# Performance work log

Measured on AMD Instinct MI355X. Metric: run time of the kernel, lower is better.

## Reference

```python
import jax, jax.numpy as jnp
import numpy as np
import math

D = 512      # d_model = sd_dim*2
DFF = 512    # dim_feedforward
S = 512      # num_seg (queries)
T = 32768    # video frames (keys)
RATE = 4     # self-attention band half-width
SCALE = 1.0 / math.sqrt(D)


def _ln(x, g, b):
    m = x.mean(-1, keepdims=True)
    v = ((x - m) ** 2).mean(-1, keepdims=True)
    return (x - m) / jnp.sqrt(v + 1e-5) * g + b


def setup_inputs() -> dict:
    key = jax.random.key(0)
    ks = jax.random.split(key, 12)
    w = lambda k, shp, s=0.02: jax.random.normal(k, shp, jnp.float32) * s
    # exactly S contiguous action segments over T frames
    action_idx = jnp.asarray((np.arange(T) * S) // T, dtype=jnp.int32)
    return dict(
        tgt=w(ks[0], (S, 1, D), 1.0), memory=w(ks[1], (T, 1, D), 1.0),
        pos=w(ks[2], (T, 1, D), 0.1), query_pos=w(ks[3], (S, 1, D), 0.1),
        action_idx=action_idx,
        ca_t2l_w=w(ks[4], (D, D)), ca_t2l_b=jnp.zeros(D),
        ca_l1_w=w(ks[5], (DFF, D)), ca_l1_b=jnp.zeros(DFF),
        ca_l2_w=w(ks[6], (D, DFF)), ca_l2_b=jnp.zeros(D),
        ca_n2_g=jnp.ones(D), ca_n2_b=jnp.zeros(D),
        ca_n3_g=jnp.ones(D), ca_n3_b=jnp.zeros(D),
        sa_conv_w=w(ks[7], (D, D)), sa_conv_b=jnp.zeros(D),
        sa_l1_w=w(ks[8], (DFF, D)), sa_l1_b=jnp.zeros(DFF),
        sa_l2_w=w(ks[9], (D, DFF)), sa_l2_b=jnp.zeros(D),
        sa_n1_g=jnp.ones(D), sa_n1_b=jnp.zeros(D),
        sa_n2_g=jnp.ones(D), sa_n2_b=jnp.zeros(D),
    )


def reference(tgt, memory, pos, query_pos, action_idx,
              ca_t2l_w, ca_t2l_b, ca_l1_w, ca_l1_b, ca_l2_w, ca_l2_b,
              ca_n2_g, ca_n2_b, ca_n3_g, ca_n3_b,
              sa_conv_w, sa_conv_b, sa_l1_w, sa_l1_b, sa_l2_w, sa_l2_b,
              sa_n1_g, sa_n1_b, sa_n2_g, sa_n2_b):
    # ---------------- CrossAttention (segment mask) ----------------
    q = tgt + query_pos                      # (S,1,D)
    k = memory + pos                         # (T,1,D)
    scores = jnp.einsum('sbd,tbd->bst', q, k) * SCALE   # (1,S,T)
    # segment id per frame from change points of action_idx
    chg = (action_idx[1:] != action_idx[:-1]).astype(jnp.int32)
    seg_id = jnp.concatenate([jnp.zeros(1, jnp.int32), jnp.cumsum(chg)])  # (T,)
    # query i attends to segments i-1, i, i+1
    mask = jnp.abs(seg_id[None, :] - jnp.arange(S, dtype=jnp.int32)[:, None]) <= 1  # (S,T)
    scores = jnp.where(mask[None], scores, -jnp.inf)
    attn = jax.nn.softmax(scores, axis=-1)               # (1,S,T)
    tgt2 = jnp.einsum('bst,tbd->sbd', attn, memory)      # (S,1,D)
    tgt2 = jnp.maximum(tgt2, 0.0) @ ca_t2l_w.T + ca_t2l_b
    x = _ln(tgt + tgt2, ca_n2_g, ca_n2_b)
    ffn = jnp.maximum(x @ ca_l1_w.T + ca_l1_b, 0.0) @ ca_l2_w.T + ca_l2_b
    x = _ln(x + ffn, ca_n3_g, ca_n3_b)                   # (S,1,D)
    # ---------------- SelfAttention (banded, pos=None) ----------------
    src = jnp.transpose(x, (1, 0, 2))                    # (1,S,D)
    s2 = jnp.einsum('bsd,btd->bst', src, src) * SCALE    # (1,S,S)
    i = jnp.arange(S)
    band = jnp.abs(i[:, None] - i[None, :]) <= RATE      # (S,S)
    s2 = jnp.where(band[None], s2, -jnp.inf)
    a2 = jax.nn.softmax(s2, axis=-1)                     # (1,S,S)
    src2 = jnp.einsum('bqk,bkd->bqd', a2, src)           # (1,S,D)
    src2 = jnp.maximum(src2, 0.0) @ sa_conv_w.T + sa_conv_b  # 1x1 conv over channels
    y = _ln(src + src2, sa_n1_g, sa_n1_b)
    ffn2 = jnp.maximum(y @ sa_l1_w.T + sa_l1_b, 0.0) @ sa_l2_w.T + sa_l2_b
    y = _ln(y + ffn2, sa_n2_g, sa_n2_b)
    return y                                              # (1,S,D)
```

## Files before the change

kernel.cpp:

```cpp
#include <hip/hip_runtime.h>

#define S_Q 512
#define DIM 512
#define SCALE_F 0.04419417382415922f

typedef short short8 __attribute__((ext_vector_type(8)));
typedef float floatx4 __attribute__((ext_vector_type(4)));

__device__ __forceinline__ float wave_reduce_sum(float v) {
#pragma unroll
  for (int off = 32; off > 0; off >>= 1) v += __shfl_xor(v, off);
  return v;
}

__device__ __forceinline__ unsigned short f2bf(float f) {
  unsigned int u = __float_as_uint(f);
  return (unsigned short)((u + 0x7FFFu + ((u >> 16) & 1u)) >> 16);
}

__global__ __launch_bounds__(256) void k_ca_partial(
    const float* __restrict__ tgt, const float* __restrict__ qpos,
    const float* __restrict__ mem, const float* __restrict__ pos,
    float* __restrict__ part_acc, float* __restrict__ part_ms) {
  const int j = blockIdx.x >> 1;
  const int h = blockIdx.x & 1;
  const int tid = threadIdx.x;
  const int wave = tid >> 6, lane = tid & 63;
  const int d0 = lane * 8;

  __shared__ float wacc[4][3][DIM];
  __shared__ float wms[4][3][2];

  float qf[3][8];
#pragma unroll
  for (int c = 0; c < 3; ++c) {
    const int qi = j - 1 + c;
    if ((unsigned)qi < (unsigned)S_Q) {
      const float4* tp = (const float4*)(tgt + (size_t)qi * DIM + d0);
      const float4* qp = (const float4*)(qpos + (size_t)qi * DIM + d0);
      float4 t0 = tp[0], t1 = tp[1], q0 = qp[0], q1 = qp[1];
      qf[c][0] = t0.x + q0.x; qf[c][1] = t0.y + q0.y;
      qf[c][2] = t0.z + q0.z; qf[c][3] = t0.w + q0.w;
      qf[c][4] = t1.x + q1.x; qf[c][5] = t1.y + q1.y;
      qf[c][6] = t1.z + q1.z; qf[c][7] = t1.w + q1.w;
    } else {
#pragma unroll
      for (int e = 0; e < 8; ++e) qf[c][e] = 0.f;
    }
  }

  float m[3] = {-1e30f, -1e30f, -1e30f};
  float ssum[3] = {0.f, 0.f, 0.f};
  float acc[3][8];
#pragma unroll
  for (int c = 0; c < 3; ++c)
#pragma unroll
    for (int e = 0; e < 8; ++e) acc[c][e] = 0.f;

  const size_t fbase = (size_t)j * 64 + h * 32 + wave * 8;
#pragma unroll 2
  for (int it = 0; it < 8; ++it) {
    const size_t f = fbase + it;
    const float4* mp = (const float4*)(mem + f * DIM + d0);
    const float4* pp = (const float4*)(pos + f * DIM + d0);
    float4 m0 = mp[0], m1 = mp[1], p0 = pp[0], p1 = pp[1];
    float mv[8] = {m0.x, m0.y, m0.z, m0.w, m1.x, m1.y, m1.z, m1.w};
    float kk[8] = {m0.x + p0.x, m0.y + p0.y, m0.z + p0.z, m0.w + p0.w,
                   m1.x + p1.x, m1.y + p1.y, m1.z + p1.z, m1.w + p1.w};
    float s0 = 0.f, s1 = 0.f, s2 = 0.f;
#pragma unroll
    for (int e = 0; e < 8; ++e) {
      s0 += qf[0][e] * kk[e];
      s1 += qf[1][e] * kk[e];
      s2 += qf[2][e] * kk[e];
    }
#pragma unroll
    for (int off = 32; off > 0; off >>= 1) {
      s0 += __shfl_xor(s0, off);
      s1 += __shfl_xor(s1, off);
      s2 += __shfl_xor(s2, off);
    }
    const float sc3[3] = {s0 * SCALE_F, s1 * SCALE_F, s2 * SCALE_F};
#pragma unroll
    for (int c = 0; c < 3; ++c) {
      const float s = sc3[c];
      if (s > m[c]) {
        const float fct = __expf(m[c] - s);
        ssum[c] = ssum[c] * fct + 1.f;
#pragma unroll
        for (int e = 0; e < 8; ++e) acc[c][e] = acc[c][e] * fct + mv[e];
        m[c] = s;
      } else {
        const float ee = __expf(s - m[c]);
        ssum[c] += ee;
#pragma unroll
        for (int e = 0; e < 8; ++e) acc[c][e] += ee * mv[e];
      }
    }
  }

#pragma unroll
  for (int c = 0; c < 3; ++c) {
    *(float4*)(&wacc[wave][c][d0]) =
        make_float4(acc[c][0], acc[c][1], acc[c][2], acc[c][3]);
    *(float4*)(&wacc[wave][c][d0 + 4]) =
        make_float4(acc[c][4], acc[c][5], acc[c][6], acc[c][7]);
    if (lane == 0) { wms[wave][c][0] = m[c]; wms[wave][c][1] = ssum[c]; }
  }
  __syncthreads();

  const int d = tid * 2;
#pragma unroll
  for (int c = 0; c < 3; ++c) {
    const int qi = j - 1 + c;
    if ((unsigned)qi >= (unsigned)S_Q) continue;
    float M = wms[0][c][0];
#pragma unroll
    for (int w = 1; w < 4; ++w) M = fmaxf(M, wms[w][c][0]);
    float S = 0.f, ax = 0.f, ay = 0.f;
#pragma unroll
    for (int w = 0; w < 4; ++w) {
      const float wgt = __expf(wms[w][c][0] - M);
      S += wgt * wms[w][c][1];
      const float2 a = *(const float2*)(&wacc[w][c][d]);
      ax += wgt * a.x;
      ay += wgt * a.y;
    }
    const size_t slot = (size_t)qi * 6 + c * 2 + h;
    *(float2*)(part_acc + slot * DIM + d) = make_float2(ax, ay);
    if (tid == 0) {
      part_ms[slot * 2 + 0] = M;
      part_ms[slot * 2 + 1] = S;
    }
  }
}

__global__ __launch_bounds__(256) void k_ca_combine(
    const float* __restrict__ part_acc, const float* __restrict__ part_ms,
    float* __restrict__ t2r) {
  const int i = blockIdx.x;
  const int tid = threadIdx.x;
  const bool valid[3] = {i < S_Q - 1, true, i > 0};
  float ms[6], ss[6];
  float M = -1e30f;
#pragma unroll
  for (int k = 0; k < 6; ++k) {
    if (valid[k >> 1]) {
      ms[k] = part_ms[((size_t)i * 6 + k) * 2 + 0];
      ss[k] = part_ms[((size_t)i * 6 + k) * 2 + 1];
      M = fmaxf(M, ms[k]);
    } else {
      ms[k] = -1e30f;
      ss[k] = 0.f;
    }
  }
  float wgt[6];
  float den = 0.f;
#pragma unroll
  for (int k = 0; k < 6; ++k) {
    wgt[k] = valid[k >> 1] ? __expf(ms[k] - M) : 0.f;
    den += wgt[k] * ss[k];
  }
  const float inv = 1.f / den;
  const int d = tid * 2;
  float ox = 0.f, oy = 0.f;
#pragma unroll
  for (int k = 0; k < 6; ++k) {
    if (valid[k >> 1]) {
      const float2 a = *(const float2*)(part_acc + ((size_t)i * 6 + k) * DIM + d);
      ox += wgt[k] * a.x;
      oy += wgt[k] * a.y;
    }
  }
  ox = fmaxf(ox * inv, 0.f);
  oy = fmaxf(oy * inv, 0.f);
  *(float2*)(t2r + (size_t)i * DIM + d) = make_float2(ox, oy);
}

template <bool RELU>
__global__ __launch_bounds__(256) void k_gemm512(
    const float* __restrict__ A, const float* __restrict__ W,
    const float* __restrict__ bias, float* __restrict__ C) {
  __shared__ short As[32 * 72];
  __shared__ short Ws[32 * 72];
  const int tid = threadIdx.x;
  const int bx = blockIdx.x, by = blockIdx.y;
  const int wave = tid >> 6, lane = tid & 63;
  const int srow = tid >> 3, sk = (tid & 7) * 4;
  const float* Ag = A + (size_t)(by * 32 + srow) * DIM + sk;
  const float* Wg = W + (size_t)(bx * 32 + srow) * DIM + sk;
  const int r0 = (wave >> 1) * 16, c0 = (wave & 1) * 16;
  const int frow = lane & 15, fk = (lane >> 4) * 8;
  floatx4 acc = {0.f, 0.f, 0.f, 0.f};
  for (int kc = 0; kc < DIM; kc += 32) {
    const float4 av = *(const float4*)(Ag + kc);
    const float4 wv = *(const float4*)(Wg + kc);
    __syncthreads();
    short* ap = &As[srow * 72 + sk];
    ap[0] = (short)f2bf(av.x); ap[1] = (short)f2bf(av.y);
    ap[2] = (short)f2bf(av.z); ap[3] = (short)f2bf(av.w);
    short* wp = &Ws[srow * 72 + sk];
    wp[0] = (short)f2bf(wv.x); wp[1] = (short)f2bf(wv.y);
    wp[2] = (short)f2bf(wv.z); wp[3] = (short)f2bf(wv.w);
    __syncthreads();
    const short8 af = *(const short8*)(&As[(r0 + frow) * 72 + fk]);
    const short8 wf = *(const short8*)(&Ws[(c0 + frow) * 72 + fk]);
    acc = __builtin_amdgcn_mfma_f32_16x16x32_bf16(af, wf, acc, 0, 0, 0);
  }
  const int col = bx * 32 + c0 + (lane & 15);
  const int rowb = by * 32 + r0 + (lane >> 4) * 4;
  const float b = bias[col];
#pragma unroll
  for (int r = 0; r < 4; ++r) {
    float val = acc[r] + b;
    if (RELU) val = fmaxf(val, 0.f);
    C[(size_t)(rowb + r) * DIM + col] = val;
  }
}

__global__ __launch_bounds__(256) void k_addln(
    const float* __restrict__ X, const float* __restrict__ R,
    const float* __restrict__ g, const float* __restrict__ b,
    float* __restrict__ out) {
  const int row = blockIdx.x * 4 + (threadIdx.x >> 6);
  const int lane = threadIdx.x & 63;
  const int d = lane * 8;
  const float4* xp = (const float4*)(X + (size_t)row * DIM + d);
  const float4* rp = (const float4*)(R + (size_t)row * DIM + d);
  float4 x0 = xp[0], x1 = xp[1], r0 = rp[0], r1 = rp[1];
  float v[8] = {x0.x + r0.x, x0.y + r0.y, x0.z + r0.z, x0.w + r0.w,
                x1.x + r1.x, x1.y + r1.y, x1.z + r1.z, x1.w + r1.w};
  float s = 0.f, sq = 0.f;
#pragma unroll
  for (int e = 0; e < 8; ++e) { s += v[e]; sq += v[e] * v[e]; }
  s = wave_reduce_sum(s);
  sq = wave_reduce_sum(sq);
  const float mean = s * (1.f / DIM);
  const float var = sq * (1.f / DIM) - mean * mean;
  const float rstd = rsqrtf(var + 1e-5f);
  const float4* gp = (const float4*)(g + d);
  const float4* bp = (const float4*)(b + d);
  float4 g0 = gp[0], g1 = gp[1], bb0 = bp[0], bb1 = bp[1];
  float4 o0, o1;
  o0.x = (v[0] - mean) * rstd * g0.x + bb0.x;
  o0.y = (v[1] - mean) * rstd * g0.y + bb0.y;
  o0.z = (v[2] - mean) * rstd * g0.z + bb0.z;
  o0.w = (v[3] - mean) * rstd * g0.w + bb0.w;
  o1.x = (v[4] - mean) * rstd * g1.x + bb1.x;
  o1.y = (v[5] - mean) * rstd * g1.y + bb1.y;
  o1.z = (v[6] - mean) * rstd * g1.z + bb1.z;
  o1.w = (v[7] - mean) * rstd * g1.w + bb1.w;
  *(float4*)(out + (size_t)row * DIM + d) = o0;
  *(float4*)(out + (size_t)row * DIM + d + 4) = o1;
}

__global__ __launch_bounds__(256) void k_sa_attn(const float* __restrict__ X,
                                                 float* __restrict__ outr) {
  const int i = blockIdx.x;
  const int tid = threadIdx.x;
  const int wave = tid >> 6, lane = tid & 63;
  const int jlo = (i - 4 > 0) ? i - 4 : 0;
  const int jhi = (i + 4 < S_Q - 1) ? i + 4 : S_Q - 1;
  const int n = jhi - jlo + 1;
  __shared__ float sc[9];
  const int d0 = lane * 8;
  const float4* qp = (const float4*)(X + (size_t)i * DIM + d0);
  float4 q0 = qp[0], q1 = qp[1];
  for (int idx = wave; idx < n; idx += 4) {
    const float4* kp = (const float4*)(X + (size_t)(jlo + idx) * DIM + d0);
    float4 k0 = kp[0], k1 = kp[1];
    float s = q0.x * k0.x + q0.y * k0.y + q0.z * k0.z + q0.w * k0.w +
              q1.x * k1.x + q1.y * k1.y + q1.z * k1.z + q1.w * k1.w;
    s = wave_reduce_sum(s);
    if (lane == 0) sc[idx] = s * SCALE_F;
  }
  __syncthreads();
  float m = -3.0e38f;
#pragma unroll
  for (int k = 0; k < 9; ++k)
    if (k < n) m = fmaxf(m, sc[k]);
  float p[9];
  float den = 0.f;
#pragma unroll
  for (int k = 0; k < 9; ++k) {
    p[k] = (k < n) ? __expf(sc[k] - m) : 0.f;
    den += p[k];
  }
  const float inv = 1.f / den;
  const int d = tid * 2;
  float ox = 0.f, oy = 0.f;
#pragma unroll
  for (int k = 0; k < 9; ++k) {
    if (k < n) {
      float2 xv = *(const float2*)(X + (size_t)(jlo + k) * DIM + d);
      ox += p[k] * xv.x;
      oy += p[k] * xv.y;
    }
  }
  ox = fmaxf(ox * inv, 0.f);
  oy = fmaxf(oy * inv, 0.f);
  *(float2*)(outr + (size_t)i * DIM + d) = make_float2(ox, oy);
}

extern "C" void kernel_launch(void* const* d_in, const int* in_sizes, int n_in,
                              void* d_out, int out_size, void* d_ws, size_t ws_size,
                              hipStream_t stream) {
  const float* tgt       = (const float*)d_in[0];
  const float* memory    = (const float*)d_in[1];
  const float* pos       = (const float*)d_in[2];
  const float* qpos      = (const float*)d_in[3];
  const float* ca_t2l_w  = (const float*)d_in[5];
  const float* ca_t2l_b  = (const float*)d_in[6];
  const float* ca_l1_w   = (const float*)d_in[7];
  const float* ca_l1_b   = (const float*)d_in[8];
  const float* ca_l2_w   = (const float*)d_in[9];
  const float* ca_l2_b   = (const float*)d_in[10];
  const float* ca_n2_g   = (const float*)d_in[11];
  const float* ca_n2_b   = (const float*)d_in[12];
  const float* ca_n3_g   = (const float*)d_in[13];
  const float* ca_n3_b   = (const float*)d_in[14];
  const float* sa_conv_w = (const float*)d_in[15];
  const float* sa_conv_b = (const float*)d_in[16];
  const float* sa_l1_w   = (const float*)d_in[17];
  const float* sa_l1_b   = (const float*)d_in[18];
  const float* sa_l2_w   = (const float*)d_in[19];
  const float* sa_l2_b   = (const float*)d_in[20];
  const float* sa_n1_g   = (const float*)d_in[21];
  const float* sa_n1_b   = (const float*)d_in[22];
  const float* sa_n2_g   = (const float*)d_in[23];
  const float* sa_n2_b   = (const float*)d_in[24];
  float* out = (float*)d_out;
  float* ws = (float*)d_ws;

  float* part_acc = ws;
  float* part_ms  = ws + 1572864;
  float* bufA     = ws + 1579008;
  float* buf1     = ws;
  float* buf2     = ws + 262144;
  float* buf3     = ws + 524288;

  const dim3 gg(16, 16, 1);

  k_ca_partial<<<1024, 256, 0, stream>>>(tgt, qpos, memory, pos, part_acc, part_ms);
  k_ca_combine<<<512, 256, 0, stream>>>(part_acc, part_ms, bufA);
  k_gemm512<false><<<gg, 256, 0, stream>>>(bufA, ca_t2l_w, ca_t2l_b, buf1);
  k_addln<<<128, 256, 0, stream>>>(buf1, tgt, ca_n2_g, ca_n2_b, buf2);
  k_gemm512<true><<<gg, 256, 0, stream>>>(buf2, ca_l1_w, ca_l1_b, bufA);
  k_gemm512<false><<<gg, 256, 0, stream>>>(bufA, ca_l2_w, ca_l2_b, buf1);
  k_addln<<<128, 256, 0, stream>>>(buf1, buf2, ca_n3_g, ca_n3_b, buf3);
  k_sa_attn<<<512, 256, 0, stream>>>(buf3, bufA);
  k_gemm512<false><<<gg, 256, 0, stream>>>(bufA, sa_conv_w, sa_conv_b, buf1);
  k_addln<<<128, 256, 0, stream>>>(buf1, buf3, sa_n1_g, sa_n1_b, buf2);
  k_gemm512<true><<<gg, 256, 0, stream>>>(buf2, sa_l1_w, sa_l1_b, bufA);
  k_gemm512<false><<<gg, 256, 0, stream>>>(bufA, sa_l2_w, sa_l2_b, buf1);
  k_addln<<<128, 256, 0, stream>>>(buf1, buf2, sa_n2_g, sa_n2_b, out);
}
```

Baseline: 300.1 us.

## Fuse combine, layernorm and banded attention into GEMM prologues; batch cross-attention softmax

Cross-attention partials now cover a whole 64-frame block per workgroup and process frames four at a time, doing one online-softmax rescale per group instead of a branch per frame. Partial accumulators are stored as bf16. The combine step, the add+layernorm steps and the banded self-attention are folded into the prologues of the following GEMMs, each of which stages its full K=512 tile in LDS once, with no per-chunk syncs. This cuts the launch count from 13 to 8 and removes several fp32 intermediate round trips. The cost is redundant layernorm and attention work repeated across the 16 column blocks, a larger LDS footprint per block, and lower precision in the partials.

Result: faster. 292.1 us (-2.7%).

```diff
diff --git a/kernel.cpp b/kernel.cpp
--- a/kernel.cpp
+++ b/kernel.cpp
@@ -3,31 +3,32 @@
 #define S_Q 512
 #define DIM 512
 #define SCALE_F 0.04419417382415922f
+#define LDS_W 520
 
 typedef short short8 __attribute__((ext_vector_type(8)));
 typedef float floatx4 __attribute__((ext_vector_type(4)));
 
-__device__ __forceinline__ float wave_reduce_sum(float v) {
-#pragma unroll
-  for (int off = 32; off > 0; off >>= 1) v += __shfl_xor(v, off);
+__device__ __forceinline__ float wave_sum(float v) {
+#pragma unroll
+  for (int o = 32; o > 0; o >>= 1) v += __shfl_xor(v, o);
   return v;
 }
-
 __device__ __forceinline__ unsigned short f2bf(float f) {
-  unsigned int u = __float_as_uint(f);
+  unsigned u = __float_as_uint(f);
   return (unsigned short)((u + 0x7FFFu + ((u >> 16) & 1u)) >> 16);
+}
+__device__ __forceinline__ float bf2f(short s) {
+  return __uint_as_float(((unsigned)(unsigned short)s) << 16);
 }
 
 __global__ __launch_bounds__(256) void k_ca_partial(
     const float* __restrict__ tgt, const float* __restrict__ qpos,
     const float* __restrict__ mem, const float* __restrict__ pos,
-    float* __restrict__ part_acc, float* __restrict__ part_ms) {
-  const int j = blockIdx.x >> 1;
-  const int h = blockIdx.x & 1;
+    unsigned short* __restrict__ part_acc, float* __restrict__ part_ms) {
+  const int j = blockIdx.x;
   const int tid = threadIdx.x;
   const int wave = tid >> 6, lane = tid & 63;
   const int d0 = lane * 8;
-
   __shared__ float wacc[4][3][DIM];
   __shared__ float wms[4][3][2];
 
@@ -36,9 +37,10 @@
   for (int c = 0; c < 3; ++c) {
     const int qi = j - 1 + c;
     if ((unsigned)qi < (unsigned)S_Q) {
-      const float4* tp = (const float4*)(tgt + (size_t)qi * DIM + d0);
-      const float4* qp = (const float4*)(qpos + (size_t)qi * DIM + d0);
-      float4 t0 = tp[0], t1 = tp[1], q0 = qp[0], q1 = qp[1];
+      float4 t0 = *(const float4*)(tgt + (size_t)qi * DIM + d0);
+      float4 t1 = *(const float4*)(tgt + (size_t)qi * DIM + d0 + 4);
+      float4 q0 = *(const float4*)(qpos + (size_t)qi * DIM + d0);
+      float4 q1 = *(const float4*)(qpos + (size_t)qi * DIM + d0 + 4);
       qf[c][0] = t0.x + q0.x; qf[c][1] = t0.y + q0.y;
       qf[c][2] = t0.z + q0.z; qf[c][3] = t0.w + q0.w;
       qf[c][4] = t1.x + q1.x; qf[c][5] = t1.y + q1.y;
@@ -57,44 +59,62 @@
 #pragma unroll
     for (int e = 0; e < 8; ++e) acc[c][e] = 0.f;
 
-  const size_t fbase = (size_t)j * 64 + h * 32 + wave * 8;
-#pragma unroll 2
-  for (int it = 0; it < 8; ++it) {
-    const size_t f = fbase + it;
-    const float4* mp = (const float4*)(mem + f * DIM + d0);
-    const float4* pp = (const float4*)(pos + f * DIM + d0);
-    float4 m0 = mp[0], m1 = mp[1], p0 = pp[0], p1 = pp[1];
-    float mv[8] = {m0.x, m0.y, m0.z, m0.w, m1.x, m1.y, m1.z, m1.w};
-    float kk[8] = {m0.x + p0.x, m0.y + p0.y, m0.z + p0.z, m0.w + p0.w,
-                   m1.x + p1.x, m1.y + p1.y, m1.z + p1.z, m1.w + p1.w};
-    float s0 = 0.f, s1 = 0.f, s2 = 0.f;
-#pragma unroll
-    for (int e = 0; e < 8; ++e) {
-      s0 += qf[0][e] * kk[e];
-      s1 += qf[1][e] * kk[e];
-      s2 += qf[2][e] * kk[e];
-    }
-#pragma unroll
-    for (int off = 32; off > 0; off >>= 1) {
-      s0 += __shfl_xor(s0, off);
-      s1 += __shfl_xor(s1, off);
-      s2 += __shfl_xor(s2, off);
-    }
-    const float sc3[3] = {s0 * SCALE_F, s1 * SCALE_F, s2 * SCALE_F};
+  const float* mbase = mem + ((size_t)j * 64 + wave * 16) * DIM + d0;
+  const float* pbase = pos + ((size_t)j * 64 + wave * 16) * DIM + d0;
+
+  for (int b = 0; b < 4; ++b) {
+    float mv[4][8], kk[4][8];
+#pragma unroll
+    for (int f = 0; f < 4; ++f) {
+      const float* mp = mbase + (size_t)(b * 4 + f) * DIM;
+      const float* pp = pbase + (size_t)(b * 4 + f) * DIM;
+      float4 a = *(const float4*)mp;
+      float4 bb = *(const float4*)(mp + 4);
+      float4 c4 = *(const float4*)pp;
+      float4 dd = *(const float4*)(pp + 4);
+      mv[f][0] = a.x;  mv[f][1] = a.y;  mv[f][2] = a.z;  mv[f][3] = a.w;
+      mv[f][4] = bb.x; mv[f][5] = bb.y; mv[f][6] = bb.z; mv[f][7] = bb.w;
+      kk[f][0] = a.x + c4.x;  kk[f][1] = a.y + c4.y;
+      kk[f][2] = a.z + c4.z;  kk[f][3] = a.w + c4.w;
+      kk[f][4] = bb.x + dd.x; kk[f][5] = bb.y + dd.y;
+      kk[f][6] = bb.z + dd.z; kk[f][7] = bb.w + dd.w;
+    }
+    float dots[3][4];
+#pragma unroll
+    for (int f = 0; f < 4; ++f) {
+      float s0 = 0.f, s1 = 0.f, s2 = 0.f;
+#pragma unroll
+      for (int e = 0; e < 8; ++e) {
+        s0 += qf[0][e] * kk[f][e];
+        s1 += qf[1][e] * kk[f][e];
+        s2 += qf[2][e] * kk[f][e];
+      }
+      dots[0][f] = s0; dots[1][f] = s1; dots[2][f] = s2;
+    }
+#pragma unroll
+    for (int o = 32; o > 0; o >>= 1)
+#pragma unroll
+      for (int c = 0; c < 3; ++c)
+#pragma unroll
+        for (int f = 0; f < 4; ++f) dots[c][f] += __shfl_xor(dots[c][f], o);
 #pragma unroll
     for (int c = 0; c < 3; ++c) {
-      const float s = sc3[c];
-      if (s > m[c]) {
-        const float fct = __expf(m[c] - s);
-        ssum[c] = ssum[c] * fct + 1.f;
-#pragma unroll
-        for (int e = 0; e < 8; ++e) acc[c][e] = acc[c][e] * fct + mv[e];
-        m[c] = s;
-      } else {
-        const float ee = __expf(s - m[c]);
-        ssum[c] += ee;
-#pragma unroll
-        for (int e = 0; e < 8; ++e) acc[c][e] += ee * mv[e];
+      float s[4];
+#pragma unroll
+      for (int f = 0; f < 4; ++f) s[f] = dots[c][f] * SCALE_F;
+      const float bm = fmaxf(fmaxf(s[0], s[1]), fmaxf(s[2], s[3]));
+      const float nm = fmaxf(m[c], bm);
+      const float fct = __expf(m[c] - nm);
+      m[c] = nm;
+      ssum[c] *= fct;
+#pragma unroll
+      for (int e = 0; e < 8; ++e) acc[c][e] *= fct;
+#pragma unroll
+      for (int f = 0; f < 4; ++f) {
+        const float w = __expf(s[f] - nm);
+        ssum[c] += w;
+#pragma unroll
+        for (int e = 0; e < 8; ++e) acc[c][e] += w * mv[f][e];
       }
     }
   }
@@ -120,14 +140,16 @@
     float S = 0.f, ax = 0.f, ay = 0.f;
 #pragma unroll
     for (int w = 0; w < 4; ++w) {
-      const float wgt = __expf(wms[w][c][0] - M);
-      S += wgt * wms[w][c][1];
+      const float wg = __expf(wms[w][c][0] - M);
+      S += wg * wms[w][c][1];
       const float2 a = *(const float2*)(&wacc[w][c][d]);
-      ax += wgt * a.x;
-      ay += wgt * a.y;
-    }
-    const size_t slot = (size_t)qi * 6 + c * 2 + h;
-    *(float2*)(part_acc + slot * DIM + d) = make_float2(ax, ay);
+      ax += wg * a.x;
+      ay += wg * a.y;
+    }
+    const size_t slot = (size_t)qi * 3 + c;
+    unsigned short* dst = part_acc + slot * DIM + d;
+    dst[0] = f2bf(ax);
+    dst[1] = f2bf(ay);
     if (tid == 0) {
       part_ms[slot * 2 + 0] = M;
       part_ms[slot * 2 + 1] = S;
@@ -135,87 +157,318 @@
   }
 }
 
-__global__ __launch_bounds__(256) void k_ca_combine(
-    const float* __restrict__ part_acc, const float* __restrict__ part_ms,
-    float* __restrict__ t2r) {
-  const int i = blockIdx.x;
-  const int tid = threadIdx.x;
-  const bool valid[3] = {i < S_Q - 1, true, i > 0};
-  float ms[6], ss[6];
-  float M = -1e30f;
-#pragma unroll
-  for (int k = 0; k < 6; ++k) {
-    if (valid[k >> 1]) {
-      ms[k] = part_ms[((size_t)i * 6 + k) * 2 + 0];
-      ss[k] = part_ms[((size_t)i * 6 + k) * 2 + 1];
-      M = fmaxf(M, ms[k]);
-    } else {
-      ms[k] = -1e30f;
-      ss[k] = 0.f;
-    }
-  }
-  float wgt[6];
-  float den = 0.f;
-#pragma unroll
-  for (int k = 0; k < 6; ++k) {
-    wgt[k] = valid[k >> 1] ? __expf(ms[k] - M) : 0.f;
-    den += wgt[k] * ss[k];
-  }
-  const float inv = 1.f / den;
-  const int d = tid * 2;
-  float ox = 0.f, oy = 0.f;
-#pragma unroll
-  for (int k = 0; k < 6; ++k) {
-    if (valid[k >> 1]) {
-      const float2 a = *(const float2*)(part_acc + ((size_t)i * 6 + k) * DIM + d);
-      ox += wgt[k] * a.x;
-      oy += wgt[k] * a.y;
-    }
-  }
-  ox = fmaxf(ox * inv, 0.f);
-  oy = fmaxf(oy * inv, 0.f);
-  *(float2*)(t2r + (size_t)i * DIM + d) = make_float2(ox, oy);
+__device__ __forceinline__ void stage_tile(const float* __restrict__ G,
+                                           short* __restrict__ Ls,
+                                           int rowblk, int tid) {
+  const int row = tid >> 3;
+  const int c0 = (tid & 7) * 64;
+  const float* src = G + (size_t)(rowblk * 32 + row) * DIM + c0;
+  short* dst = &Ls[row * LDS_W + c0];
+#pragma unroll
+  for (int u = 0; u < 8; ++u) {
+    float4 a = *(const float4*)(src + u * 8);
+    float4 b = *(const float4*)(src + u * 8 + 4);
+    short8 s;
+    s[0] = (short)f2bf(a.x); s[1] = (short)f2bf(a.y);
+    s[2] = (short)f2bf(a.z); s[3] = (short)f2bf(a.w);
+    s[4] = (short)f2bf(b.x); s[5] = (short)f2bf(b.y);
+    s[6] = (short)f2bf(b.z); s[7] = (short)f2bf(b.w);
+    *(short8*)(dst + u * 8) = s;
+  }
 }
 
 template <bool RELU>
-__global__ __launch_bounds__(256) void k_gemm512(
-    const float* __restrict__ A, const float* __restrict__ W,
+__device__ __forceinline__ void gemm_core(const short* __restrict__ As,
+                                          const short* __restrict__ Ws,
+                                          const float* __restrict__ bias,
+                                          float* __restrict__ C, int bx, int by,
+                                          int wave, int lane) {
+  const int r0 = (wave >> 1) * 16, c0 = (wave & 1) * 16;
+  const int frow = lane & 15, fk = (lane >> 4) * 8;
+  const short* ap = &As[(r0 + frow) * LDS_W + fk];
+  const short* wp = &Ws[(c0 + frow) * LDS_W + fk];
+  floatx4 acc = {0.f, 0.f, 0.f, 0.f};
+#pragma unroll
+  for (int kc = 0; kc < 16; ++kc) {
+    const short8 af = *(const short8*)(ap + kc * 32);
+    const short8 wf = *(const short8*)(wp + kc * 32);
+    acc = __builtin_amdgcn_mfma_f32_16x16x32_bf16(af, wf, acc, 0, 0, 0);
+  }
+  const int col = bx * 32 + c0 + frow;
+  const int rowb = by * 32 + r0 + (lane >> 4) * 4;
+  const float b = bias[col];
+#pragma unroll
+  for (int r = 0; r < 4; ++r) {
+    float v = acc[r] + b;
+    if (RELU) v = fmaxf(v, 0.f);
+    C[(size_t)(rowb + r) * DIM + col] = v;
+  }
+}
+
+__device__ __forceinline__ void ln_prologue(const float* __restrict__ X,
+                                            const float* __restrict__ R,
+                                            const float* __restrict__ g,
+                                            const float* __restrict__ b,
+                                            short* __restrict__ As, int by,
+                                            float* x_out, int wave, int lane) {
+  const int d0 = lane * 8;
+  float gg[8], bb[8];
+  {
+    float4 g0 = *(const float4*)(g + d0);
+    float4 g1 = *(const float4*)(g + d0 + 4);
+    float4 b0 = *(const float4*)(b + d0);
+    float4 b1 = *(const float4*)(b + d0 + 4);
+    gg[0] = g0.x; gg[1] = g0.y; gg[2] = g0.z; gg[3] = g0.w;
+    gg[4] = g1.x; gg[5] = g1.y; gg[6] = g1.z; gg[7] = g1.w;
+    bb[0] = b0.x; bb[1] = b0.y; bb[2] = b0.z; bb[3] = b0.w;
+    bb[4] = b1.x; bb[5] = b1.y; bb[6] = b1.z; bb[7] = b1.w;
+  }
+  for (int r = wave; r < 32; r += 4) {
+    const int grow = by * 32 + r;
+    const float* xp = X + (size_t)grow * DIM + d0;
+    const float* rp = R + (size_t)grow * DIM + d0;
+    float4 x0 = *(const float4*)xp;
+    float4 x1 = *(const float4*)(xp + 4);
+    float4 r0 = *(const float4*)rp;
+    float4 r1 = *(const float4*)(rp + 4);
+    float v[8] = {x0.x + r0.x, x0.y + r0.y, x0.z + r0.z, x0.w + r0.w,
+                  x1.x + r1.x, x1.y + r1.y, x1.z + r1.z, x1.w + r1.w};
+    float s = 0.f, sq = 0.f;
+#pragma unroll
+    for (int e = 0; e < 8; ++e) { s += v[e]; sq += v[e] * v[e]; }
+#pragma unroll
+    for (int o = 32; o > 0; o >>= 1) {
+      s += __shfl_xor(s, o);
+      sq += __shfl_xor(sq, o);
+    }
+    const float mean = s * (1.f / DIM);
+    const float var = sq * (1.f / DIM) - mean * mean;
+    const float rstd = rsqrtf(var + 1e-5f);
+    float o8[8];
+    short8 sv;
+#pragma unroll
+    for (int e = 0; e < 8; ++e) {
+      o8[e] = (v[e] - mean) * rstd * gg[e] + bb[e];
+      sv[e] = (short)f2bf(o8[e]);
+    }
+    *(short8*)(&As[r * LDS_W + d0]) = sv;
+    if (x_out) {
+      *(float4*)(x_out + (size_t)grow * DIM + d0) =
+          make_float4(o8[0], o8[1], o8[2], o8[3]);
+      *(float4*)(x_out + (size_t)grow * DIM + d0 + 4) =
+          make_float4(o8[4], o8[5], o8[6], o8[7]);
+    }
+  }
+}
+
+__global__ __launch_bounds__(256) void k_g1(
+    const unsigned short* __restrict__ part_acc,
+    const float* __restrict__ part_ms, const float* __restrict__ W,
     const float* __restrict__ bias, float* __restrict__ C) {
-  __shared__ short As[32 * 72];
-  __shared__ short Ws[32 * 72];
+  __shared__ short As[32 * LDS_W];
+  __shared__ short Ws[32 * LDS_W];
   const int tid = threadIdx.x;
   const int bx = blockIdx.x, by = blockIdx.y;
   const int wave = tid >> 6, lane = tid & 63;
-  const int srow = tid >> 3, sk = (tid & 7) * 4;
-  const float* Ag = A + (size_t)(by * 32 + srow) * DIM + sk;
-  const float* Wg = W + (size_t)(bx * 32 + srow) * DIM + sk;
-  const int r0 = (wave >> 1) * 16, c0 = (wave & 1) * 16;
-  const int frow = lane & 15, fk = (lane >> 4) * 8;
-  floatx4 acc = {0.f, 0.f, 0.f, 0.f};
-  for (int kc = 0; kc < DIM; kc += 32) {
-    const float4 av = *(const float4*)(Ag + kc);
-    const float4 wv = *(const float4*)(Wg + kc);
-    __syncthreads();
-    short* ap = &As[srow * 72 + sk];
-    ap[0] = (short)f2bf(av.x); ap[1] = (short)f2bf(av.y);
-    ap[2] = (short)f2bf(av.z); ap[3] = (short)f2bf(av.w);
-    short* wp = &Ws[srow * 72 + sk];
-    wp[0] = (short)f2bf(wv.x); wp[1] = (short)f2bf(wv.y);
-    wp[2] = (short)f2bf(wv.z); wp[3] = (short)f2bf(wv.w);
-    __syncthreads();
-    const short8 af = *(const short8*)(&As[(r0 + frow) * 72 + fk]);
-    const short8 wf = *(const short8*)(&Ws[(c0 + frow) * 72 + fk]);
-    acc = __builtin_amdgcn_mfma_f32_16x16x32_bf16(af, wf, acc, 0, 0, 0);
-  }
-  const int col = bx * 32 + c0 + (lane & 15);
-  const int rowb = by * 32 + r0 + (lane >> 4) * 4;
-  const float b = bias[col];
-#pragma unroll
-  for (int r = 0; r < 4; ++r) {
-    float val = acc[r] + b;
-    if (RELU) val = fmaxf(val, 0.f);
-    C[(size_t)(rowb + r) * DIM + col] = val;
-  }
+  const int d0 = lane * 8;
+  for (int r = wave; r < 32; r += 4) {
+    const int i = by * 32 + r;
+    const bool valid[3] = {i < S_Q - 1, true, i > 0};
+    float mm[3], ss[3], M = -1e30f;
+#pragma unroll
+    for (int c = 0; c < 3; ++c) {
+      if (valid[c]) {
+        mm[c] = part_ms[((size_t)i * 3 + c) * 2 + 0];
+        ss[c] = part_ms[((size_t)i * 3 + c) * 2 + 1];
+        M = fmaxf(M, mm[c]);
+      } else {
+        mm[c] = -1e30f;
+        ss[c] = 0.f;
+      }
+    }
+    float den = 0.f, wg[3];
+#pragma unroll
+    for (int c = 0; c < 3; ++c) {
+      wg[c] = valid[c] ? __expf(mm[c] - M) : 0.f;
+      den += wg[c] * ss[c];
+    }
+    const float inv = 1.f / den;
+    float o[8] = {0.f, 0.f, 0.f, 0.f, 0.f, 0.f, 0.f, 0.f};
+#pragma unroll
+    for (int c = 0; c < 3; ++c) {
+      if (valid[c]) {
+        const short8 pa =
+            *(const short8*)(part_acc + ((size_t)i * 3 + c) * DIM + d0);
+#pragma unroll
+        for (int e = 0; e < 8; ++e) o[e] += wg[c] * bf2f(pa[e]);
+      }
+    }
+    short8 sv;
+#pragma unroll
+    for (int e = 0; e < 8; ++e) sv[e] = (short)f2bf(fmaxf(o[e] * inv, 0.f));
+    *(short8*)(&As[r * LDS_W + d0]) = sv;
+  }
+  stage_tile(W, Ws, bx, tid);
+  __syncthreads();
+  gemm_core<false>(As, Ws, bias, C, bx, by, wave, lane);
+}
+
+__global__ __launch_bounds__(256) void k_gln(
+    const float* __restrict__ X, const float* __restrict__ R,
+    const float* __restrict__ g, const float* __restrict__ b,
+    const float* __restrict__ W, const float* __restrict__ bias,
+    float* __restrict__ C, float* __restrict__ x_out) {
+  __shared__ short As[32 * LDS_W];
+  __shared__ short Ws[32 * LDS_W];
+  const int tid = threadIdx.x;
+  const int bx = blockIdx.x, by = blockIdx.y;
+  const int wave = tid >> 6, lane = tid & 63;
+  ln_prologue(X, R, g, b, As, by, (bx == 0) ? x_out : nullptr, wave, lane);
+  stage_tile(W, Ws, bx, tid);
+  __syncthreads();
+  gemm_core<true>(As, Ws, bias, C, bx, by, wave, lane);
+}
+
+__global__ __launch_bounds__(256) void k_gplain(
+    const float* __restrict__ A, const float* __restrict__ W,
+    const float* __restrict__ bias, float* __restrict__ C) {
+  __shared__ short As[32 * LDS_W];
+  __shared__ short Ws[32 * LDS_W];
+  const int tid = threadIdx.x;
+  const int bx = blockIdx.x, by = blockIdx.y;
+  const int wave = tid >> 6, lane = tid & 63;
+  stage_tile(A, As, by, tid);
+  stage_tile(W, Ws, bx, tid);
+  __syncthreads();
+  gemm_core<false>(As, Ws, bias, C, bx, by, wave, lane);
+}
+
+__global__ __launch_bounds__(256) void k_g4(
+    const float* __restrict__ X, const float* __restrict__ R,
+    const float* __restrict__ g, const float* __restrict__ b,
+    const float* __restrict__ W, const float* __restrict__ bias,
+    float* __restrict__ C, float* __restrict__ x2_out) {
+  __shared__ short Xw[40 * LDS_W];
+  __shared__ short As[32 * LDS_W];
+  __shared__ short Ws[32 * LDS_W];
+  const int tid = threadIdx.x;
+  const int bx = blockIdx.x, by = blockIdx.y;
+  const int wave = tid >> 6, lane = tid & 63;
+  const int d0 = lane * 8;
+  const int wlo = (by * 32 - 4 > 0) ? by * 32 - 4 : 0;
+  const int whi = (by * 32 + 35 < S_Q - 1) ? by * 32 + 35 : S_Q - 1;
+  const int nw = whi - wlo + 1;
+
+  {
+    float gg[8], bb[8];
+    float4 g0 = *(const float4*)(g + d0);
+    float4 g1 = *(const float4*)(g + d0 + 4);
+    float4 b0 = *(const float4*)(b + d0);
+    float4 b1 = *(const float4*)(b + d0 + 4);
+    gg[0] = g0.x; gg[1] = g0.y; gg[2] = g0.z; gg[3] = g0.w;
+    gg[4] = g1.x; gg[5] = g1.y; gg[6] = g1.z; gg[7] = g1.w;
+    bb[0] = b0.x; bb[1] = b0.y; bb[2] = b0.z; bb[3] = b0.w;
+    bb[4] = b1.x; bb[5] = b1.y; bb[6] = b1.z; bb[7] = b1.w;
+    for (int r = wave; r < nw; r += 4) {
+      const int grow = wlo + r;
+      const float* xp = X + (size_t)grow * DIM + d0;
+      const float* rp = R + (size_t)grow * DIM + d0;
+      float4 x0 = *(const float4*)xp;
+      float4 x1 = *(const float4*)(xp + 4);
+      float4 r0 = *(const float4*)rp;
+      float4 r1 = *(const float4*)(rp + 4);
+      float v[8] = {x0.x + r0.x, x0.y + r0.y, x0.z + r0.z, x0.w + r0.w,
+                    x1.x + r1.x, x1.y + r1.y, x1.z + r1.z, x1.w + r1.w};
+      float s = 0.f, sq = 0.f;
+#pragma unroll
+      for (int e = 0; e < 8; ++e) { s += v[e]; sq += v[e] * v[e]; }
+#pragma unroll
+      for (int o = 32; o > 0; o >>= 1) {
+        s += __shfl_xor(s, o);
+        sq += __shfl_xor(sq, o);
+      }
+      const float mean = s * (1.f / DIM);
+      const float var = sq * (1.f / DIM) - mean * mean;
+      const float rstd = rsqrtf(var + 1e-5f);
+      float o8[8];
+      short8 sv;
+#pragma unroll
+      for (int e = 0; e < 8; ++e) {
+        o8[e] = (v[e] - mean) * rstd * gg[e] + bb[e];
+        sv[e] = (short)f2bf(o8[e]);
+      }
+      *(short8*)(&Xw[r * LDS_W + d0]) = sv;
+      if (bx == 0 && grow >= by * 32 && grow < by * 32 + 32) {
+        *(float4*)(x2_out + (size_t)grow * DIM + d0) =
+            make_float4(o8[0], o8[1], o8[2], o8[3]);
+        *(float4*)(x2_out + (size_t)grow * DIM + d0 + 4) =
+            make_float4(o8[4], o8[5], o8[6], o8[7]);
+      }
+    }
+  }
+  stage_tile(W, Ws, bx, tid);
+  __syncthreads();
+
+  for (int li = wave; li < 32; li += 4) {
+    const int i = by * 32 + li;
+    const int lq = i - wlo;
+    float qv[8];
+    {
+      const short8 qs = *(const short8*)(&Xw[lq * LDS_W + d0]);
+#pragma unroll
+      for (int e = 0; e < 8; ++e) qv[e] = bf2f(qs[e]);
+    }
+    const int jlo = (i - 4 > 0) ? i - 4 : 0;
+    const int jhi = (i + 4 < S_Q - 1) ? i + 4 : S_Q - 1;
+    const int n = jhi - jlo + 1;
+    float sc[9];
+#pragma unroll
+    for (int k = 0; k < 9; ++k) {
+      if (k < n) {
+        const int lk = jlo + k - wlo;
+        const short8 ks = *(const short8*)(&Xw[lk * LDS_W + d0]);
+        float dd = 0.f;
+#pragma unroll
+        for (int e = 0; e < 8; ++e) dd += qv[e] * bf2f(ks[e]);
+        sc[k] = dd;
+      } else {
+        sc[k] = 0.f;
+      }
+    }
+#pragma unroll
+    for (int o = 32; o > 0; o >>= 1)
+#pragma unroll
+      for (int k = 0; k < 9; ++k) sc[k] += __shfl_xor(sc[k], o);
+    float M = -1e30f;
+#pragma unroll
+    for (int k = 0; k < 9; ++k) {
+      sc[k] *= SCALE_F;
+      if (k < n) M = fmaxf(M, sc[k]);
+    }
+    float p[9], den = 0.f;
+#pragma unroll
+    for (int k = 0; k < 9; ++k) {
+      p[k] = (k < n) ? __expf(sc[k] - M) : 0.f;
+      den += p[k];
+    }
+    const float inv = 1.f / den;
+    float o8[8] = {0.f, 0.f, 0.f, 0.f, 0.f, 0.f, 0.f, 0.f};
+#pragma unroll
+    for (int k = 0; k < 9; ++k) {
+      if (k < n) {
+        const int lk = jlo + k - wlo;
+        const short8 ks = *(const short8*)(&Xw[lk * LDS_W + d0]);
+#pragma unroll
+        for (int e = 0; e < 8; ++e) o8[e] += p[k] * bf2f(ks[e]);
+      }
+    }
+    short8 sv;
+#pragma unroll
+    for (int e = 0; e < 8; ++e) sv[e] = (short)f2bf(fmaxf(o8[e] * inv, 0.f));
+    *(short8*)(&As[li * LDS_W + d0]) = sv;
+  }
+  __syncthreads();
+  gemm_core<false>(As, Ws, bias, C, bx, by, wave, lane);
 }
 
 __global__ __launch_bounds__(256) void k_addln(
@@ -233,8 +486,8 @@
   float s = 0.f, sq = 0.f;
 #pragma unroll
   for (int e = 0; e < 8; ++e) { s += v[e]; sq += v[e] * v[e]; }
-  s = wave_reduce_sum(s);
-  sq = wave_reduce_sum(sq);
+  s = wave_sum(s);
+  sq = wave_sum(sq);
   const float mean = s * (1.f / DIM);
   const float var = sq * (1.f / DIM) - mean * mean;
   const float rstd = rsqrtf(var + 1e-5f);
@@ -252,54 +505,6 @@
   o1.w = (v[7] - mean) * rstd * g1.w + bb1.w;
   *(float4*)(out + (size_t)row * DIM + d) = o0;
   *(float4*)(out + (size_t)row * DIM + d + 4) = o1;
-}
-
-__global__ __launch_bounds__(256) void k_sa_attn(const float* __restrict__ X,
-                                                 float* __restrict__ outr) {
-  const int i = blockIdx.x;
-  const int tid = threadIdx.x;
-  const int wave = tid >> 6, lane = tid & 63;
-  const int jlo = (i - 4 > 0) ? i - 4 : 0;
-  const int jhi = (i + 4 < S_Q - 1) ? i + 4 : S_Q - 1;
-  const int n = jhi - jlo + 1;
-  __shared__ float sc[9];
-  const int d0 = lane * 8;
-  const float4* qp = (const float4*)(X + (size_t)i * DIM + d0);
-  float4 q0 = qp[0], q1 = qp[1];
-  for (int idx = wave; idx < n; idx += 4) {
-    const float4* kp = (const float4*)(X + (size_t)(jlo + idx) * DIM + d0);
-    float4 k0 = kp[0], k1 = kp[1];
-    float s = q0.x * k0.x + q0.y * k0.y + q0.z * k0.z + q0.w * k0.w +
-              q1.x * k1.x + q1.y * k1.y + q1.z * k1.z + q1.w * k1.w;
-    s = wave_reduce_sum(s);
-    if (lane == 0) sc[idx] = s * SCALE_F;
-  }
-  __syncthreads();
-  float m = -3.0e38f;
-#pragma unroll
-  for (int k = 0; k < 9; ++k)
-    if (k < n) m = fmaxf(m, sc[k]);
-  float p[9];
-  float den = 0.f;
-#pragma unroll
-  for (int k = 0; k < 9; ++k) {
-    p[k] = (k < n) ? __expf(sc[k] - m) : 0.f;
-    den += p[k];
-  }
-  const float inv = 1.f / den;
-  const int d = tid * 2;
-  float ox = 0.f, oy = 0.f;
-#pragma unroll
-  for (int k = 0; k < 9; ++k) {
-    if (k < n) {
-      float2 xv = *(const float2*)(X + (size_t)(jlo + k) * DIM + d);
-      ox += p[k] * xv.x;
-      oy += p[k] * xv.y;
-    }
-  }
-  ox = fmaxf(ox * inv, 0.f);
-  oy = fmaxf(oy * inv, 0.f);
-  *(float2*)(outr + (size_t)i * DIM + d) = make_float2(ox, oy);
 }
 
 extern "C" void kernel_launch(void* const* d_in, const int* in_sizes, int n_in,
@@ -332,26 +537,26 @@
   float* out = (float*)d_out;
   float* ws = (float*)d_ws;
 
-  float* part_acc = ws;
-  float* part_ms  = ws + 1572864;
-  float* bufA     = ws + 1579008;
-  float* buf1     = ws;
-  float* buf2     = ws + 262144;
-  float* buf3     = ws + 524288;
+  unsigned short* part_acc = (unsigned short*)ws;
+  float* part_ms = ws + 393216;
+  float* t2 = ws + 396288;
+  float* h  = ws + 658432;
+  float* x  = ws + 920576;
+  float* f  = ws + 0;
+  float* x2 = ws + 396288;
+  float* c  = ws + 658432;
+  float* y1 = ws + 0;
+  float* h2 = ws + 920576;
+  float* f2 = ws + 396288;
 
   const dim3 gg(16, 16, 1);
 
-  k_ca_partial<<<1024, 256, 0, stream>>>(tgt, qpos, memory, pos, part_acc, part_ms);
-  k_ca_combine<<<512, 256, 0, stream>>>(part_acc, part_ms, bufA);
-  k_gemm512<false><<<gg, 256, 0, stream>>>(bufA, ca_t2l_w, ca_t2l_b, buf1);
-  k_addln<<<128, 256, 0, stream>>>(buf1, tgt, ca_n2_g, ca_n2_b, buf2);
-  k_gemm512<true><<<gg, 256, 0, stream>>>(buf2, ca_l1_w, ca_l1_b, bufA);
-  k_gemm512<false><<<gg, 256, 0, stream>>>(bufA, ca_l2_w, ca_l2_b, buf1);
-  k_addln<<<128, 256, 0, stream>>>(buf1, buf2, ca_n3_g, ca_n3_b, buf3);
-  k_sa_attn<<<512, 256, 0, stream>>>(buf3, bufA);
-  k_gemm512<false><<<gg, 256, 0, stream>>>(bufA, sa_conv_w, sa_conv_b, buf1);
-  k_addln<<<128, 256, 0, stream>>>(buf1, buf3, sa_n1_g, sa_n1_b, buf2);
-  k_gemm512<true><<<gg, 256, 0, stream>>>(buf2, sa_l1_w, sa_l1_b, bufA);
-  k_gemm512<false><<<gg, 256, 0, stream>>>(bufA, sa_l2_w, sa_l2_b, buf1);
-  k_addln<<<128, 256, 0, stream>>>(buf1, buf2, sa_n2_g, sa_n2_b, out);
-}
+  k_ca_partial<<<512, 256, 0, stream>>>(tgt, qpos, memory, pos, part_acc, part_ms);
+  k_g1<<<gg, 256, 0, stream>>>(part_acc, part_ms, ca_t2l_w, ca_t2l_b, t2);
+  k_gln<<<gg, 256, 0, stream>>>(tgt, t2, ca_n2_g, ca_n2_b, ca_l1_w, ca_l1_b, h, x);
+  k_gplain<<<gg, 256, 0, stream>>>(h, ca_l2_w, ca_l2_b, f);
+  k_g4<<<gg, 256, 0, stream>>>(x, f, ca_n3_g, ca_n3_b, sa_conv_w, sa_conv_b, c, x2);
+  k_gln<<<gg, 256, 0, stream>>>(x2, c, sa_n1_g, sa_n1_b, sa_l1_w, sa_l1_b, h2, y1);
+  k_gplain<<<gg, 256, 0, stream>>>(h2, sa_l2_w, sa_l2_b, f2);
+  k_addln<<<128, 256, 0, stream>>>(f2, y1, sa_n2_g, sa_n2_b, out);
+}
```
